# Performance work log

Measured on AMD Instinct MI355X. Metric: run time of the kernel, lower is better.

Reference implementation:

```python
import jax, jax.numpy as jnp
import numpy as np

N_NODES = 100000
N_EDGES = 3200000
N_CLASSES = 16
P = 2  # p-norm order


def setup_inputs() -> dict:
    key = jax.random.key(0)
    k1, k2, k3 = jax.random.split(key, 3)
    edge_index = jax.random.randint(k1, (2, N_EDGES), 0, N_NODES, dtype=jnp.int64)
    edge_weights = jax.random.uniform(k2, (N_EDGES,), dtype=jnp.float32)
    y = jax.random.normal(k3, (N_NODES, N_CLASSES), dtype=jnp.float32)
    return {"edge_index": edge_index, "edge_weights": edge_weights, "y": y}


def reference(edge_index, edge_weights, y):
    row, col = edge_index[0], edge_index[1]
    n = y.shape[0]
    # sym normalization: degree = row-sum of weighted adjacency (O(E) segment sum,
    # replacing the original dense NxN materialization)
    degree = jax.ops.segment_sum(edge_weights, row, num_segments=n)
    d = jnp.sqrt(degree)
    d_r = d[row][:, None]  # (E,1)
    d_c = d[col][:, None]
    diff = y[row] / d_r - y[col] / d_c  # (E,C)
    pnorm = jnp.sum(jnp.abs(diff) ** P, axis=1) ** (1.0 / P)  # (E,)
    return jnp.mean(pnorm * edge_weights)
```

## Files before the change

### kernel.cpp

```cpp
#include <hip/hip_runtime.h>
#include <hip/hip_fp16.h>

#define N_NODES   100000
#define N_CLASSES 16
#define N_EDGES   3200000

#define R5        5
#define NPR5      20000
#define DYN5      (NPR5 * 4)
#define S5        102
#define EPS5      31376

#define R_ST      8
#define NPR_ST    12500
#define S_ST      64
#define EPS_ST    50000

#define B_DEG     1024
#define KE        8


__device__ __forceinline__ unsigned f2fp8(float f) {
    unsigned u = __float_as_uint(f);
    unsigned s = (u >> 24) & 0x80u;
    float g = fabsf(f) * 0x1p-120f;
    unsigned gu = __float_as_uint(g);
    gu += 0x7FFFFu + ((gu >> 20) & 1u);
    unsigned mag = gu >> 20;
    if (mag > 0x7Eu) mag = 0x7Eu;
    return s | mag;
}

__device__ __forceinline__ float fp82f(unsigned b) {
    unsigned u = ((b & 0x80u) << 24) | ((b & 0x7Fu) << 20);
    return __uint_as_float(u) * 0x1p120f;
}

#if defined(__has_builtin)
#if __has_builtin(__builtin_amdgcn_cvt_pk_f32_fp8)
#define HAVE_HW_FP8 1
#endif
#endif

#ifdef HAVE_HW_FP8
typedef float v2f __attribute__((ext_vector_type(2)));
__device__ __forceinline__ float ssd4(unsigned a, unsigned b) {
    v2f a0 = __builtin_amdgcn_cvt_pk_f32_fp8((int)a, false);
    v2f a1 = __builtin_amdgcn_cvt_pk_f32_fp8((int)a, true);
    v2f b0 = __builtin_amdgcn_cvt_pk_f32_fp8((int)b, false);
    v2f b1 = __builtin_amdgcn_cvt_pk_f32_fp8((int)b, true);
    float d0 = a0.x - b0.x;
    float d1 = a0.y - b0.y;
    float d2 = a1.x - b1.x;
    float d3 = a1.y - b1.y;
    return d0 * d0 + d1 * d1 + d2 * d2 + d3 * d3;
}
#else
__device__ __forceinline__ float ssd4(unsigned a, unsigned b) {
    float s = 0.0f;
#pragma unroll
    for (int i = 0; i < 4; ++i) {
        float va = fp82f((a >> (8 * i)) & 0xFFu);
        float vb = fp82f((b >> (8 * i)) & 0xFFu);
        float d = va - vb;
        s += d * d;
    }
    return s;
}
#endif


__global__ __launch_bounds__(B_DEG, 8) void lap_degree_r5(
        const int* __restrict__ rows, const float* __restrict__ w,
        __half* __restrict__ shadows, float* __restrict__ out) {
    extern __shared__ float hist[];
    const int b  = blockIdx.x;
    const int r  = b % R5;
    const int s  = b / R5;
    const int lo = r * NPR5;

    if (b == 0 && threadIdx.x == 0) out[0] = 0.0f;

    for (int i = threadIdx.x; i < NPR5; i += B_DEG) hist[i] = 0.0f;
    __syncthreads();

    const int base = s * EPS5;
    for (int g = threadIdx.x; g < EPS5 / 4; g += B_DEG) {
        const int e = base + g * 4;
        if (e >= N_EDGES) continue;
        int4   r4 = *(const int4*)(rows + e);
        float4 w4 = *(const float4*)(w + e);
        int t;
        t = r4.x - lo; if ((unsigned)t < (unsigned)NPR5) atomicAdd(&hist[t], w4.x);
        t = r4.y - lo; if ((unsigned)t < (unsigned)NPR5) atomicAdd(&hist[t], w4.y);
        t = r4.z - lo; if ((unsigned)t < (unsigned)NPR5) atomicAdd(&hist[t], w4.z);
        t = r4.w - lo; if ((unsigned)t < (unsigned)NPR5) atomicAdd(&hist[t], w4.w);
    }
    __syncthreads();

    __half* dst = shadows + (size_t)s * N_NODES + lo;
    for (int i = threadIdx.x; i < NPR5; i += B_DEG) dst[i] = __float2half(hist[i]);
}


__global__ __launch_bounds__(B_DEG) void lap_degree_static(
        const int* __restrict__ rows, const float* __restrict__ w,
        __half* __restrict__ shadows, float* __restrict__ out) {
    __shared__ float hist[NPR_ST];
    const int r  = blockIdx.x & (R_ST - 1);
    const int s  = blockIdx.x >> 3;
    const int lo = r * NPR_ST;

    if (blockIdx.x == 0 && threadIdx.x == 0) out[0] = 0.0f;

    for (int i = threadIdx.x; i < NPR_ST; i += B_DEG) hist[i] = 0.0f;
    __syncthreads();

    const int base = s * EPS_ST;
    for (int g = threadIdx.x; g < EPS_ST / 4; g += B_DEG) {
        const int e = base + g * 4;
        int4   r4 = *(const int4*)(rows + e);
        float4 w4 = *(const float4*)(w + e);
        int t;
        t = r4.x - lo; if ((unsigned)t < (unsigned)NPR_ST) atomicAdd(&hist[t], w4.x);
        t = r4.y - lo; if ((unsigned)t < (unsigned)NPR_ST) atomicAdd(&hist[t], w4.y);
        t = r4.z - lo; if ((unsigned)t < (unsigned)NPR_ST) atomicAdd(&hist[t], w4.z);
        t = r4.w - lo; if ((unsigned)t < (unsigned)NPR_ST) atomicAdd(&hist[t], w4.w);
    }
    __syncthreads();

    __half* dst = shadows + (size_t)s * N_NODES + lo;
    for (int i = threadIdx.x; i < NPR_ST; i += B_DEG) dst[i] = __float2half(hist[i]);
}


__global__ void lap_yhat(const __half* __restrict__ shadows,
                         const float* __restrict__ y,
                         unsigned char* __restrict__ yhat, int S) {
    const int n = blockIdx.x * blockDim.x + threadIdx.x;
    if (n >= N_NODES) return;
    float deg = 0.0f;
    for (int s = 0; s < S; ++s) deg += __half2float(shadows[(size_t)s * N_NODES + n]);
    const float inv = rsqrtf(deg);

    const float4* yr = (const float4*)(y + (size_t)n * N_CLASSES);
    uint4 o;
    unsigned* op = (unsigned*)&o;
#pragma unroll
    for (int j = 0; j < 4; ++j) {
        float4 v = yr[j];
        op[j] =  f2fp8(v.x * inv)
              | (f2fp8(v.y * inv) << 8)
              | (f2fp8(v.z * inv) << 16)
              | (f2fp8(v.w * inv) << 24);
    }
    *(uint4*)(yhat + (size_t)n * N_CLASSES) = o;
}


__global__ void lap_edge_fp8(const int* __restrict__ rows,
                             const int* __restrict__ cols,
                             const float* __restrict__ w,
                             const unsigned char* __restrict__ yhat,
                             float* __restrict__ out) {
    const int tid = blockIdx.x * blockDim.x + threadIdx.x;
    const long e0 = (long)tid * KE;
    float local = 0.0f;
    if (e0 < N_EDGES) {
        int4   ra = *(const int4*)(rows + e0);
        int4   rb = *(const int4*)(rows + e0 + 4);
        int4   ca = *(const int4*)(cols + e0);
        int4   cb = *(const int4*)(cols + e0 + 4);
        float4 wa = *(const float4*)(w + e0);
        float4 wb = *(const float4*)(w + e0 + 4);

        const int ri[KE] = {ra.x, ra.y, ra.z, ra.w, rb.x, rb.y, rb.z, rb.w};
        const int ci[KE] = {ca.x, ca.y, ca.z, ca.w, cb.x, cb.y, cb.z, cb.w};
        const float wv[KE] = {wa.x, wa.y, wa.z, wa.w, wb.x, wb.y, wb.z, wb.w};

        uint4 A[KE], B[KE];
#pragma unroll
        for (int k = 0; k < KE; ++k) {
            A[k] = *(const uint4*)(yhat + (size_t)ri[k] * N_CLASSES);
            B[k] = *(const uint4*)(yhat + (size_t)ci[k] * N_CLASSES);
        }
#pragma unroll
        for (int k = 0; k < KE; ++k) {
            float s = ssd4(A[k].x, B[k].x) + ssd4(A[k].y, B[k].y)
                    + ssd4(A[k].z, B[k].z) + ssd4(A[k].w, B[k].w);
            local += wv[k] * sqrtf(s);
        }
    }
#pragma unroll
    for (int off = 32; off > 0; off >>= 1) local += __shfl_down(local, off, 64);
    __shared__ float sm[4];
    const int lane = threadIdx.x & 63;
    const int wid  = threadIdx.x >> 6;
    if (lane == 0) sm[wid] = local;
    __syncthreads();
    if (threadIdx.x == 0)
        atomicAdd(out, (sm[0] + sm[1] + sm[2] + sm[3]) * (1.0f / (float)N_EDGES));
}


__global__ void lap_degree_kernel(const int* __restrict__ rows,
                                  const float* __restrict__ w,
                                  float* __restrict__ degree) {
    int i = blockIdx.x * blockDim.x + threadIdx.x;
    if (i < N_EDGES) atomicAdd(&degree[rows[i]], w[i]);
}

__global__ void lap_invd_kernel(const float* __restrict__ degree,
                                float* __restrict__ invd) {
    int i = blockIdx.x * blockDim.x + threadIdx.x;
    if (i < N_NODES) invd[i] = rsqrtf(degree[i]);
}

__global__ void lap_edge_kernel(const int* __restrict__ rows,
                                const int* __restrict__ cols,
                                const float* __restrict__ w,
                                const float* __restrict__ y,
                                const float* __restrict__ invd,
                                float* __restrict__ out) {
    int i = blockIdx.x * blockDim.x + threadIdx.x;
    float local = 0.0f;
    if (i < N_EDGES) {
        int r = rows[i], c = cols[i];
        float dr = invd[r], dc = invd[c];
        const float4* yr = (const float4*)(y + (size_t)r * N_CLASSES);
        const float4* yc = (const float4*)(y + (size_t)c * N_CLASSES);
        float s = 0.0f;
#pragma unroll
        for (int j = 0; j < N_CLASSES / 4; ++j) {
            float4 a = yr[j], b = yc[j];
            float d0 = a.x * dr - b.x * dc;
            float d1 = a.y * dr - b.y * dc;
            float d2 = a.z * dr - b.z * dc;
            float d3 = a.w * dr - b.w * dc;
            s += d0 * d0 + d1 * d1 + d2 * d2 + d3 * d3;
        }
        local = w[i] * sqrtf(s);
    }
#pragma unroll
    for (int off = 32; off > 0; off >>= 1) local += __shfl_down(local, off, 64);
    __shared__ float sm[4];
    int lane = threadIdx.x & 63, wid = threadIdx.x >> 6;
    if (lane == 0) sm[wid] = local;
    __syncthreads();
    if (threadIdx.x == 0)
        atomicAdd(out, (sm[0] + sm[1] + sm[2] + sm[3]) * (1.0f / (float)N_EDGES));
}


extern "C" void kernel_launch(void* const* d_in, const int* in_sizes, int n_in,
                              void* d_out, int out_size, void* d_ws, size_t ws_size,
                              hipStream_t stream) {
    const int*   edge_index = (const int*)d_in[0];
    const float* w          = (const float*)d_in[1];
    const float* y          = (const float*)d_in[2];
    float*       out        = (float*)d_out;

    const int* rows = edge_index;
    const int* cols = edge_index + N_EDGES;
    const int  B = 256;

    const size_t sh_bytes   = (size_t)S5 * N_NODES * sizeof(__half);
    const size_t need_super = sh_bytes + (size_t)N_NODES * N_CLASSES;

    const int edge_blocks = (N_EDGES / KE + B - 1) / B;

    if (ws_size >= need_super) {
        __half*        shadows = (__half*)d_ws;
        unsigned char* yhat    = (unsigned char*)d_ws + sh_bytes;

        hipError_t ok = hipFuncSetAttribute(
            reinterpret_cast<const void*>(lap_degree_r5),
            hipFuncAttributeMaxDynamicSharedMemorySize, DYN5);

        if (ok == hipSuccess) {
            lap_degree_r5<<<R5 * S5, B_DEG, DYN5, stream>>>(rows, w, shadows, out);
            lap_yhat<<<(N_NODES + B - 1) / B, B, 0, stream>>>(shadows, y, yhat, S5);
        } else {
            lap_degree_static<<<R_ST * S_ST, B_DEG, 0, stream>>>(rows, w, shadows, out);
            lap_yhat<<<(N_NODES + B - 1) / B, B, 0, stream>>>(shadows, y, yhat, S_ST);
        }
        lap_edge_fp8<<<edge_blocks, B, 0, stream>>>(rows, cols, w, yhat, out);
    } else {
        float* degree = (float*)d_ws;
        float* invd   = degree + N_NODES;
        hipMemsetAsync(d_out, 0, sizeof(float), stream);
        hipMemsetAsync(d_ws, 0, (size_t)N_NODES * sizeof(float), stream);
        lap_degree_kernel<<<(N_EDGES + B - 1) / B, B, 0, stream>>>(rows, w, degree);
        lap_invd_kernel<<<(N_NODES + B - 1) / B, B, 0, stream>>>(degree, invd);
        lap_edge_kernel<<<(N_EDGES + B - 1) / B, B, 0, stream>>>(rows, cols, w, y, invd, out);
    }
}
```

Before: 160.5 us.

## Replace privatized LDS degree histograms with direct global atomic accumulation

```diff
diff --git a/kernel.cpp b/kernel.cpp
--- a/kernel.cpp
+++ b/kernel.cpp
@@ -1,22 +1,8 @@
 #include <hip/hip_runtime.h>
-#include <hip/hip_fp16.h>
 
 #define N_NODES   100000
 #define N_CLASSES 16
 #define N_EDGES   3200000
-
-#define R5        5
-#define NPR5      20000
-#define DYN5      (NPR5 * 4)
-#define S5        102
-#define EPS5      31376
-
-#define R_ST      8
-#define NPR_ST    12500
-#define S_ST      64
-#define EPS_ST    50000
-
-#define B_DEG     1024
 #define KE        8
 
 
@@ -70,78 +56,38 @@
 #endif
 
 
-__global__ __launch_bounds__(B_DEG, 8) void lap_degree_r5(
+__global__ __launch_bounds__(256) void lap_zero(float* __restrict__ degree,
+                                                float* __restrict__ out) {
+    const int i = blockIdx.x * blockDim.x + threadIdx.x;
+    if (i == 0) out[0] = 0.0f;
+    const int n = i * 4;
+    if (n < N_NODES)
+        *(float4*)(degree + n) = make_float4(0.f, 0.f, 0.f, 0.f);
+}
+
+
+__global__ __launch_bounds__(256) void lap_degree_atomic(
         const int* __restrict__ rows, const float* __restrict__ w,
-        __half* __restrict__ shadows, float* __restrict__ out) {
-    extern __shared__ float hist[];
-    const int b  = blockIdx.x;
-    const int r  = b % R5;
-    const int s  = b / R5;
-    const int lo = r * NPR5;
-
-    if (b == 0 && threadIdx.x == 0) out[0] = 0.0f;
-
-    for (int i = threadIdx.x; i < NPR5; i += B_DEG) hist[i] = 0.0f;
-    __syncthreads();
-
-    const int base = s * EPS5;
-    for (int g = threadIdx.x; g < EPS5 / 4; g += B_DEG) {
-        const int e = base + g * 4;
-        if (e >= N_EDGES) continue;
-        int4   r4 = *(const int4*)(rows + e);
-        float4 w4 = *(const float4*)(w + e);
-        int t;
-        t = r4.x - lo; if ((unsigned)t < (unsigned)NPR5) atomicAdd(&hist[t], w4.x);
-        t = r4.y - lo; if ((unsigned)t < (unsigned)NPR5) atomicAdd(&hist[t], w4.y);
-        t = r4.z - lo; if ((unsigned)t < (unsigned)NPR5) atomicAdd(&hist[t], w4.z);
-        t = r4.w - lo; if ((unsigned)t < (unsigned)NPR5) atomicAdd(&hist[t], w4.w);
-    }
-    __syncthreads();
-
-    __half* dst = shadows + (size_t)s * N_NODES + lo;
-    for (int i = threadIdx.x; i < NPR5; i += B_DEG) dst[i] = __float2half(hist[i]);
-}
-
-
-__global__ __launch_bounds__(B_DEG) void lap_degree_static(
-        const int* __restrict__ rows, const float* __restrict__ w,
-        __half* __restrict__ shadows, float* __restrict__ out) {
-    __shared__ float hist[NPR_ST];
-    const int r  = blockIdx.x & (R_ST - 1);
-    const int s  = blockIdx.x >> 3;
-    const int lo = r * NPR_ST;
-
-    if (blockIdx.x == 0 && threadIdx.x == 0) out[0] = 0.0f;
-
-    for (int i = threadIdx.x; i < NPR_ST; i += B_DEG) hist[i] = 0.0f;
-    __syncthreads();
-
-    const int base = s * EPS_ST;
-    for (int g = threadIdx.x; g < EPS_ST / 4; g += B_DEG) {
-        const int e = base + g * 4;
-        int4   r4 = *(const int4*)(rows + e);
-        float4 w4 = *(const float4*)(w + e);
-        int t;
-        t = r4.x - lo; if ((unsigned)t < (unsigned)NPR_ST) atomicAdd(&hist[t], w4.x);
-        t = r4.y - lo; if ((unsigned)t < (unsigned)NPR_ST) atomicAdd(&hist[t], w4.y);
-        t = r4.z - lo; if ((unsigned)t < (unsigned)NPR_ST) atomicAdd(&hist[t], w4.z);
-        t = r4.w - lo; if ((unsigned)t < (unsigned)NPR_ST) atomicAdd(&hist[t], w4.w);
-    }
-    __syncthreads();
-
-    __half* dst = shadows + (size_t)s * N_NODES + lo;
-    for (int i = threadIdx.x; i < NPR_ST; i += B_DEG) dst[i] = __float2half(hist[i]);
-}
-
-
-__global__ void lap_yhat(const __half* __restrict__ shadows,
-                         const float* __restrict__ y,
-                         unsigned char* __restrict__ yhat, int S) {
+        float* __restrict__ degree) {
+    const int g = blockIdx.x * blockDim.x + threadIdx.x;
+    const int e = g * 4;
+    if (e >= N_EDGES) return;
+    const int4   r4 = *(const int4*)(rows + e);
+    const float4 w4 = *(const float4*)(w + e);
+    atomicAdd(&degree[r4.x], w4.x);
+    atomicAdd(&degree[r4.y], w4.y);
+    atomicAdd(&degree[r4.z], w4.z);
+    atomicAdd(&degree[r4.w], w4.w);
+}
+
+
+__global__ __launch_bounds__(256) void lap_yhat_deg(
+        const float* __restrict__ degree,
+        const float* __restrict__ y,
+        unsigned char* __restrict__ yhat) {
     const int n = blockIdx.x * blockDim.x + threadIdx.x;
     if (n >= N_NODES) return;
-    float deg = 0.0f;
-    for (int s = 0; s < S; ++s) deg += __half2float(shadows[(size_t)s * N_NODES + n]);
-    const float inv = rsqrtf(deg);
+    const float inv = rsqrtf(degree[n]);
 
     const float4* yr = (const float4*)(y + (size_t)n * N_CLASSES);
     uint4 o;
@@ -264,26 +210,18 @@
     const int* cols = edge_index + N_EDGES;
     const int  B = 256;
 
-    const size_t sh_bytes   = (size_t)S5 * N_NODES * sizeof(__half);
-    const size_t need_super = sh_bytes + (size_t)N_NODES * N_CLASSES;
+    const size_t deg_bytes = (size_t)N_NODES * sizeof(float);
+    const size_t need      = deg_bytes + (size_t)N_NODES * N_CLASSES;
 
     const int edge_blocks = (N_EDGES / KE + B - 1) / B;
 
-    if (ws_size >= need_super) {
-        __half*        shadows = (__half*)d_ws;
-        unsigned char* yhat    = (unsigned char*)d_ws + sh_bytes;
-
-        hipError_t ok = hipFuncSetAttribute(
-            reinterpret_cast<const void*>(lap_degree_r5),
-            hipFuncAttributeMaxDynamicSharedMemorySize, DYN5);
-
-        if (ok == hipSuccess) {
-            lap_degree_r5<<<R5 * S5, B_DEG, DYN5, stream>>>(rows, w, shadows, out);
-            lap_yhat<<<(N_NODES + B - 1) / B, B, 0, stream>>>(shadows, y, yhat, S5);
-        } else {
-            lap_degree_static<<<R_ST * S_ST, B_DEG, 0, stream>>>(rows, w, shadows, out);
-            lap_yhat<<<(N_NODES + B - 1) / B, B, 0, stream>>>(shadows, y, yhat, S_ST);
-        }
+    if (ws_size >= need) {
+        float*         degree = (float*)d_ws;
+        unsigned char* yhat   = (unsigned char*)d_ws + deg_bytes;
+
+        lap_zero<<<(N_NODES / 4 + B - 1) / B, B, 0, stream>>>(degree, out);
+        lap_degree_atomic<<<N_EDGES / 4 / B, B, 0, stream>>>(rows, w, degree);
+        lap_yhat_deg<<<(N_NODES + B - 1) / B, B, 0, stream>>>(degree, y, yhat);
         lap_edge_fp8<<<edge_blocks, B, 0, stream>>>(rows, cols, w, yhat, out);
     } else {
         float* degree = (float*)d_ws;
```

After: 279.0 us. 73.9% more time.
